# Optimization experiments

Hardware: AMD Instinct MI355X
Metric: run time of the kernel (lower is better)

The kernel has to match this reference:

```python
import jax, jax.numpy as jnp
import numpy as np

E = 8          # n_routed_experts
TOP_K = 2      # num_experts_per_tok
H = 1024       # hidden_size
I = 512        # moe_intermediate_size
SI = 512       # shared expert intermediate (I * n_shared_experts)
B, S = 4, 4096


def setup_inputs() -> dict:
    key = jax.random.key(0)
    ks = jax.random.split(key, 8)
    sc_h = 1.0 / np.sqrt(H)
    sc_i = 1.0 / np.sqrt(I)
    return {
        "hidden_states": jax.random.normal(ks[0], (B, S, H), jnp.float32),
        "gate_w": jax.random.normal(ks[1], (E, H), jnp.float32) * sc_h,  # router logits weight [E,H]
        "Wg": jax.random.normal(ks[2], (E, H, I), jnp.float32) * sc_h,   # per-expert gate_proj
        "Wu": jax.random.normal(ks[3], (E, H, I), jnp.float32) * sc_h,   # per-expert up_proj
        "Wd": jax.random.normal(ks[4], (E, I, H), jnp.float32) * sc_i,   # per-expert down_proj
        "sWg": jax.random.normal(ks[5], (H, SI), jnp.float32) * sc_h,    # shared expert gate_proj
        "sWu": jax.random.normal(ks[6], (H, SI), jnp.float32) * sc_h,
        "sWd": jax.random.normal(ks[7], (SI, H), jnp.float32) * sc_i,
    }


def reference(hidden_states, gate_w, Wg, Wu, Wd, sWg, sWu, sWd):
    b, s, h = hidden_states.shape
    x = hidden_states.reshape(-1, h)                      # [T,H]

    # ---- MoEGate: softmax scoring + greedy top-k + weight normalization ----
    logits = x.astype(jnp.float32) @ gate_w.T             # [T,E]
    scores = jax.nn.softmax(logits, axis=-1)
    topk_w, topk_idx = jax.lax.top_k(scores, TOP_K)       # [T,K]
    topk_w = topk_w / (topk_w.sum(-1, keepdims=True) + 1e-20)  # norm_topk_prob

    # combine weights as a dense [T,E] map (scatter of topk weights)
    cw = (jax.nn.one_hot(topk_idx, E, dtype=topk_w.dtype) * topk_w[..., None]).sum(1)  # [T,E]

    # ---- routed experts: down(gelu(gate(x)) * up(x)), combined by gate weight ----
    g = jnp.einsum("th,ehi->tei", x, Wg)
    u = jnp.einsum("th,ehi->tei", x, Wu)
    inter = jax.nn.gelu(g, approximate=False) * u         # [T,E,I]
    y = jnp.einsum("tei,te,eih->th", inter, cw.astype(x.dtype), Wd)

    # ---- shared expert on the identity path ----
    sh = (jax.nn.gelu(x @ sWg, approximate=False) * (x @ sWu)) @ sWd

    return (y + sh).reshape(b, s, h)
```

## Files before the change

kernel.cpp:

```cpp
#include <hip/hip_runtime.h>
#include <hip/hip_bf16.h>
#include <math.h>


#define T_TOTAL 16384
#define HDIM 1024
#define IDIM 512
#define NE 9
#define CNT_STRIDE 16

typedef __bf16 bf16x8 __attribute__((ext_vector_type(8)));
typedef float f32x4 __attribute__((ext_vector_type(4)));

typedef __attribute__((address_space(1))) void gvoid_t;
typedef __attribute__((address_space(3))) void lvoid_t;

__device__ __forceinline__ void load_lds16(const void* g, void* l) {
  __builtin_amdgcn_global_load_lds((const gvoid_t*)g, (lvoid_t*)l, 16, 0, 0);
}

__device__ __forceinline__ f32x4 mfma_bf16(bf16x8 a, bf16x8 b, f32x4 c) {
  return __builtin_amdgcn_mfma_f32_16x16x32_bf16(a, b, c, 0, 0, 0);
}

__global__ __launch_bounds__(256) void k_gate(const float* __restrict__ x,
                                              const float* __restrict__ gw,
                                              __bf16* __restrict__ xb,
                                              int* __restrict__ tok,
                                              float* __restrict__ wtl,
                                              int* __restrict__ cnt) {
  __shared__ int s_eid[64][2];
  __shared__ float s_wt[64][2];
  __shared__ int s_rank[64][2];
  __shared__ int lcnt[8];
  __shared__ int lbase[8];
  const int wv = threadIdx.x >> 6, lane = threadIdx.x & 63;
  if (threadIdx.x < 8) lcnt[threadIdx.x] = 0;
  __syncthreads();

  for (int i = 0; i < 16; i++) {
    const int tl = wv * 16 + i;
    const int t = blockIdx.x * 64 + tl;
    const float* xr = x + (size_t)t * HDIM + lane * 16;
    float4 xv[4];
#pragma unroll
    for (int j = 0; j < 4; j++) xv[j] = ((const float4*)xr)[j];

    bf16x8 v0, v1;
#pragma unroll
    for (int j = 0; j < 8; j++) v0[j] = (__bf16)((const float*)xv)[j];
#pragma unroll
    for (int j = 0; j < 8; j++) v1[j] = (__bf16)((const float*)xv)[j + 8];
    bf16x8* xbo = (bf16x8*)(xb + (size_t)t * HDIM + lane * 16);
    xbo[0] = v0;
    xbo[1] = v1;

    float acc[8];
#pragma unroll
    for (int e = 0; e < 8; e++) {
      const float4* gp = (const float4*)(gw + e * HDIM + lane * 16);
      float s = 0.f;
#pragma unroll
      for (int j = 0; j < 4; j++) {
        float4 g = gp[j];
        s += xv[j].x * g.x + xv[j].y * g.y + xv[j].z * g.z + xv[j].w * g.w;
      }
      acc[e] = s;
    }
#pragma unroll
    for (int d = 32; d >= 1; d >>= 1) {
#pragma unroll
      for (int e = 0; e < 8; e++) acc[e] += __shfl_xor(acc[e], d, 64);
    }
    if (lane == 0) {
      float mx = acc[0];
#pragma unroll
      for (int e = 1; e < 8; e++) mx = fmaxf(mx, acc[e]);
      float p[8], Z = 0.f;
#pragma unroll
      for (int e = 0; e < 8; e++) {
        p[e] = expf(acc[e] - mx);
        Z += p[e];
      }
#pragma unroll
      for (int e = 0; e < 8; e++) p[e] /= Z;
      int i1 = 0;
#pragma unroll
      for (int e = 1; e < 8; e++)
        if (p[e] > p[i1]) i1 = e;
      int i2 = (i1 == 0) ? 1 : 0;
#pragma unroll
      for (int e = 0; e < 8; e++)
        if (e != i1 && p[e] > p[i2]) i2 = e;
      const float s12 = p[i1] + p[i2] + 1e-20f;
      s_eid[tl][0] = i1;
      s_eid[tl][1] = i2;
      s_wt[tl][0] = p[i1] / s12;
      s_wt[tl][1] = p[i2] / s12;
    }
  }
  __syncthreads();

  if (threadIdx.x < 64) {
    s_rank[threadIdx.x][0] = atomicAdd(&lcnt[s_eid[threadIdx.x][0]], 1);
    s_rank[threadIdx.x][1] = atomicAdd(&lcnt[s_eid[threadIdx.x][1]], 1);
  }
  __syncthreads();
  if (threadIdx.x < 8)
    lbase[threadIdx.x] =
        atomicAdd(&cnt[threadIdx.x * CNT_STRIDE], lcnt[threadIdx.x]);
  __syncthreads();
  if (threadIdx.x < 64) {
    const int t = blockIdx.x * 64 + threadIdx.x;
#pragma unroll
    for (int j = 0; j < 2; j++) {
      const int e = s_eid[threadIdx.x][j];
      const int slot = lbase[e] + s_rank[threadIdx.x][j];
      tok[e * T_TOTAL + slot] = t;
      wtl[e * T_TOTAL + slot] = s_wt[threadIdx.x][j];
    }
  }
}

__global__ __launch_bounds__(256) void k_transpose(const float* __restrict__ w8,
                                                   const float* __restrict__ w1,
                                                   __bf16* __restrict__ out,
                                                   int R, int C) {
  __shared__ float tile[32][33];
  const int b = blockIdx.z;
  const float* src = (b < 8) ? (w8 + (size_t)b * R * C) : w1;
  const int c0 = blockIdx.x * 32, r0 = blockIdx.y * 32;
  const int tx = threadIdx.x & 31, ty = threadIdx.x >> 5;
#pragma unroll
  for (int i = 0; i < 4; i++)
    tile[ty + i * 8][tx] = src[(size_t)(r0 + ty + i * 8) * C + c0 + tx];
  __syncthreads();
#pragma unroll
  for (int i = 0; i < 4; i++)
    out[(size_t)b * R * C + (size_t)(c0 + ty + i * 8) * R + r0 + tx] =
        (__bf16)tile[tx][ty + i * 8];
}

__global__ __launch_bounds__(256) void k_transpose_fuse(
    const float* __restrict__ w8, const float* __restrict__ w1,
    __bf16* __restrict__ out, int u16off) {
  __shared__ float tile[32][33];
  const int b = blockIdx.z;
  const float* src = (b < 8) ? (w8 + (size_t)b * HDIM * IDIM) : w1;
  const int c0 = blockIdx.x * 32, r0 = blockIdx.y * 32;
  const int tx = threadIdx.x & 31, ty = threadIdx.x >> 5;
#pragma unroll
  for (int i = 0; i < 4; i++)
    tile[ty + i * 8][tx] = src[(size_t)(r0 + ty + i * 8) * IDIM + c0 + tx];
  __syncthreads();
#pragma unroll
  for (int i = 0; i < 4; i++) {
    const int ic = c0 + ty + i * 8;
    const int f = 2 * (ic & ~15) + (ic & 15) + u16off;
    out[(size_t)b * 1024 * HDIM + (size_t)f * HDIM + r0 + tx] =
        (__bf16)tile[tx][ty + i * 8];
  }
}

__global__ __launch_bounds__(256, 2) void k_gu(
    const __bf16* __restrict__ xb, const __bf16* __restrict__ Wfu,
    const int* __restrict__ tok, const float* __restrict__ wtl,
    const int* __restrict__ cnt, __bf16* __restrict__ inter) {
  const int e = blockIdx.z;
  const bool se = (e == 8);
  const int cnt_e = se ? T_TOTAL : cnt[e * CNT_STRIDE];
  const int m0 = blockIdx.x * 128;
  if (m0 >= cnt_e) return;

  __shared__ __bf16 sA[128][64];
  __shared__ __bf16 sB[128][64];
  const int tid = threadIdx.x, w = tid >> 6, lane = tid & 63;
  const int n0 = blockIdx.y * 128;
  const int quad = lane >> 4, l16 = lane & 15;
  const int wm = (w & 1) * 64, wn = (w >> 1) * 64;

  const int sr = tid >> 3;
  const int scs = ((tid & 7) ^ (sr & 7)) * 8;
  const __bf16* ap[4];
  const __bf16* bp[4];
#pragma unroll
  for (int sh = 0; sh < 4; sh++) {
    int s = m0 + sh * 32 + sr;
    if (s > cnt_e - 1) s = cnt_e - 1;
    const int t = se ? s : tok[e * T_TOTAL + s];
    ap[sh] = xb + (size_t)t * HDIM + scs;
    bp[sh] = Wfu + ((size_t)e * 1024 + n0 + sh * 32 + sr) * HDIM + scs;
  }
  char* const la = (char*)sA + w * 1024;
  char* const lb = (char*)sB + w * 1024;

  f32x4 acc[4][4];
#pragma unroll
  for (int im = 0; im < 4; im++)
#pragma unroll
    for (int in = 0; in < 4; in++) acc[im][in] = {0.f, 0.f, 0.f, 0.f};

  for (int k = 0; k < HDIM; k += 64) {
    __syncthreads();
#pragma unroll
    for (int sh = 0; sh < 4; sh++) {
      load_lds16(ap[sh], la + sh * 4096);
      load_lds16(bp[sh], lb + sh * 4096);
      ap[sh] += 64;
      bp[sh] += 64;
    }
    __syncthreads();
#pragma unroll
    for (int kh = 0; kh < 2; kh++) {
      bf16x8 af[4], bfr[4];
#pragma unroll
      for (int i = 0; i < 4; i++) {
        const int ra = wm + i * 16 + l16;
        af[i] = *(const bf16x8*)((const char*)sA + ra * 128 +
                                 ((kh * 4 + quad) ^ (ra & 7)) * 16);
        const int rb = wn + i * 16 + l16;
        bfr[i] = *(const bf16x8*)((const char*)sB + rb * 128 +
                                  ((kh * 4 + quad) ^ (rb & 7)) * 16);
      }
#pragma unroll
      for (int im = 0; im < 4; im++)
#pragma unroll
        for (int in = 0; in < 4; in++)
          acc[im][in] = mfma_bf16(af[im], bfr[in], acc[im][in]);
    }
  }

#pragma unroll
  for (int im = 0; im < 4; im++) {
#pragma unroll
    for (int r = 0; r < 4; r++) {
      const int slot = m0 + wm + im * 16 + quad * 4 + r;
      if (slot < cnt_e) {
        const float wt = se ? 1.0f : wtl[e * T_TOTAL + slot];
        __bf16* op =
            inter + ((size_t)e * T_TOTAL + slot) * IDIM + ((n0 + wn) >> 1) + l16;
#pragma unroll
        for (int p = 0; p < 2; p++) {
          const float g = acc[im][2 * p][r];
          const float u = acc[im][2 * p + 1][r];
          const float v =
              wt * u * 0.5f * g * (1.0f + erff(g * 0.70710678118654752f));
          op[p * 16] = (__bf16)v;
        }
      }
    }
  }
}

__global__ __launch_bounds__(256, 2) void k_down_s(const __bf16* __restrict__ iA,
                                                   const __bf16* __restrict__ wB,
                                                   float* __restrict__ out) {
  __shared__ __bf16 sA[128][64];
  __shared__ __bf16 sB[128][64];
  const int tid = threadIdx.x, w = tid >> 6, lane = tid & 63;
  const int m0 = blockIdx.x * 128, n0 = blockIdx.y * 128;
  const int quad = lane >> 4, l16 = lane & 15;
  const int wm = (w & 1) * 64, wn = (w >> 1) * 64;

  const int sr = tid >> 3;
  const int scs = ((tid & 7) ^ (sr & 7)) * 8;
  const __bf16* ap[4];
  const __bf16* bp[4];
#pragma unroll
  for (int sh = 0; sh < 4; sh++) {
    ap[sh] = iA + (size_t)(m0 + sh * 32 + sr) * IDIM + scs;
    bp[sh] = wB + (size_t)(n0 + sh * 32 + sr) * IDIM + scs;
  }
  char* const la = (char*)sA + w * 1024;
  char* const lb = (char*)sB + w * 1024;

  f32x4 acc[4][4];
#pragma unroll
  for (int im = 0; im < 4; im++)
#pragma unroll
    for (int in = 0; in < 4; in++) acc[im][in] = {0.f, 0.f, 0.f, 0.f};

  for (int k = 0; k < IDIM; k += 64) {
    __syncthreads();
#pragma unroll
    for (int sh = 0; sh < 4; sh++) {
      load_lds16(ap[sh], la + sh * 4096);
      load_lds16(bp[sh], lb + sh * 4096);
      ap[sh] += 64;
      bp[sh] += 64;
    }
    __syncthreads();
#pragma unroll
    for (int kh = 0; kh < 2; kh++) {
      bf16x8 af[4], bfr[4];
#pragma unroll
      for (int i = 0; i < 4; i++) {
        const int ra = wm + i * 16 + l16;
        af[i] = *(const bf16x8*)((const char*)sA + ra * 128 +
                                 ((kh * 4 + quad) ^ (ra & 7)) * 16);
        const int rb = wn + i * 16 + l16;
        bfr[i] = *(const bf16x8*)((const char*)sB + rb * 128 +
                                  ((kh * 4 + quad) ^ (rb & 7)) * 16);
      }
#pragma unroll
      for (int im = 0; im < 4; im++)
#pragma unroll
        for (int in = 0; in < 4; in++)
          acc[im][in] = mfma_bf16(af[im], bfr[in], acc[im][in]);
    }
  }

#pragma unroll
  for (int im = 0; im < 4; im++) {
#pragma unroll
    for (int r = 0; r < 4; r++) {
      const int t = m0 + wm + im * 16 + quad * 4 + r;
#pragma unroll
      for (int in = 0; in < 4; in++)
        out[(size_t)t * HDIM + n0 + wn + in * 16 + l16] = acc[im][in][r];
    }
  }
}

__global__ __launch_bounds__(256, 2) void k_down_r(
    const __bf16* __restrict__ inter, const __bf16* __restrict__ WdT,
    const int* __restrict__ tok, const int* __restrict__ cnt,
    float* __restrict__ out) {
  const int e = blockIdx.z;
  const int cnt_e = cnt[e * CNT_STRIDE];
  const int m0 = blockIdx.x * 128;
  if (m0 >= cnt_e) return;

  __shared__ __bf16 sA[128][64];
  __shared__ __bf16 sB[128][64];
  const int tid = threadIdx.x, w = tid >> 6, lane = tid & 63;
  const int n0 = blockIdx.y * 128;
  const int quad = lane >> 4, l16 = lane & 15;
  const int wm = (w & 1) * 64, wn = (w >> 1) * 64;

  const int sr = tid >> 3;
  const int scs = ((tid & 7) ^ (sr & 7)) * 8;
  const __bf16* ap[4];
  const __bf16* bp[4];
#pragma unroll
  for (int sh = 0; sh < 4; sh++) {
    int s = m0 + sh * 32 + sr;
    if (s > cnt_e - 1) s = cnt_e - 1;
    ap[sh] = inter + ((size_t)e * T_TOTAL + s) * IDIM + scs;
    bp[sh] = WdT + ((size_t)e * HDIM + n0 + sh * 32 + sr) * IDIM + scs;
  }
  char* const la = (char*)sA + w * 1024;
  char* const lb = (char*)sB + w * 1024;

  f32x4 acc[4][4];
#pragma unroll
  for (int im = 0; im < 4; im++)
#pragma unroll
    for (int in = 0; in < 4; in++) acc[im][in] = {0.f, 0.f, 0.f, 0.f};

  for (int k = 0; k < IDIM; k += 64) {
    __syncthreads();
#pragma unroll
    for (int sh = 0; sh < 4; sh++) {
      load_lds16(ap[sh], la + sh * 4096);
      load_lds16(bp[sh], lb + sh * 4096);
      ap[sh] += 64;
      bp[sh] += 64;
    }
    __syncthreads();
#pragma unroll
    for (int kh = 0; kh < 2; kh++) {
      bf16x8 af[4], bfr[4];
#pragma unroll
      for (int i = 0; i < 4; i++) {
        const int ra = wm + i * 16 + l16;
        af[i] = *(const bf16x8*)((const char*)sA + ra * 128 +
                                 ((kh * 4 + quad) ^ (ra & 7)) * 16);
        const int rb = wn + i * 16 + l16;
        bfr[i] = *(const bf16x8*)((const char*)sB + rb * 128 +
                                  ((kh * 4 + quad) ^ (rb & 7)) * 16);
      }
#pragma unroll
      for (int im = 0; im < 4; im++)
#pragma unroll
        for (int in = 0; in < 4; in++)
          acc[im][in] = mfma_bf16(af[im], bfr[in], acc[im][in]);
    }
  }

#pragma unroll
  for (int im = 0; im < 4; im++) {
#pragma unroll
    for (int r = 0; r < 4; r++) {
      const int slot = m0 + wm + im * 16 + quad * 4 + r;
      if (slot < cnt_e) {
        const int t = tok[e * T_TOTAL + slot];
#pragma unroll
        for (int in = 0; in < 4; in++)
          atomicAdd(&out[(size_t)t * HDIM + n0 + wn + in * 16 + l16],
                    acc[im][in][r]);
      }
    }
  }
}

extern "C" void kernel_launch(void* const* d_in, const int* in_sizes, int n_in,
                              void* d_out, int out_size, void* d_ws,
                              size_t ws_size, hipStream_t stream) {
  const float* x = (const float*)d_in[0];
  const float* gw = (const float*)d_in[1];
  const float* Wg = (const float*)d_in[2];
  const float* Wu = (const float*)d_in[3];
  const float* Wd = (const float*)d_in[4];
  const float* sWg = (const float*)d_in[5];
  const float* sWu = (const float*)d_in[6];
  const float* sWd = (const float*)d_in[7];
  float* out = (float*)d_out;

  char* ws = (char*)d_ws;
  size_t off = 0;
  auto alloc = [&](size_t n) {
    char* p = ws + off;
    off += (n + 255) & ~(size_t)255;
    return p;
  };
  __bf16* xb = (__bf16*)alloc((size_t)T_TOTAL * HDIM * 2);
  __bf16* Wfu = (__bf16*)alloc((size_t)NE * 1024 * HDIM * 2);
  __bf16* WdT = (__bf16*)alloc((size_t)NE * HDIM * IDIM * 2);
  int* tok = (int*)alloc((size_t)8 * T_TOTAL * 4);
  float* wtl = (float*)alloc((size_t)8 * T_TOTAL * 4);
  int* cnt = (int*)alloc(8 * CNT_STRIDE * 4);
  __bf16* inter = (__bf16*)alloc((size_t)NE * T_TOTAL * IDIM * 2);

  hipMemsetAsync(cnt, 0, 8 * CNT_STRIDE * 4, stream);

  k_gate<<<dim3(T_TOTAL / 64), dim3(256), 0, stream>>>(x, gw, xb, tok, wtl,
                                                       cnt);
  k_transpose_fuse<<<dim3(IDIM / 32, HDIM / 32, NE), dim3(256), 0, stream>>>(
      Wg, sWg, Wfu, 0);
  k_transpose_fuse<<<dim3(IDIM / 32, HDIM / 32, NE), dim3(256), 0, stream>>>(
      Wu, sWu, Wfu, 16);
  k_transpose<<<dim3(HDIM / 32, IDIM / 32, NE), dim3(256), 0, stream>>>(
      Wd, sWd, WdT, IDIM, HDIM);

  k_gu<<<dim3(T_TOTAL / 128, 1024 / 128, NE), dim3(256), 0, stream>>>(
      xb, Wfu, tok, wtl, cnt, inter);

  k_down_s<<<dim3(T_TOTAL / 128, HDIM / 128), dim3(256), 0, stream>>>(
      inter + (size_t)8 * T_TOTAL * IDIM, WdT + (size_t)8 * HDIM * IDIM, out);
  k_down_r<<<dim3(T_TOTAL / 128, HDIM / 128, 8), dim3(256), 0, stream>>>(
      inter, WdT, tok, cnt, out);
}
```

Baseline: 487.0 us.

## Rewrite gate/up GEMM with 256x256 tiles and 4-stage async LDS pipeline

The fused gate/up expert GEMM now uses 512-thread blocks computing 256x256 output tiles with K-step 32. A four-buffer global-to-LDS ring keeps two stages of loads in flight, waited on with explicit vmcnt and raw barriers instead of a full sync around each K step. It also adds setprio around the MFMA bursts and a new swizzle for the paired-row layout. This targets global memory latency stalls and improves operand reuse per block. In exchange it needs 128KB of LDS per block, which limits occupancy, and routed experts with few tokens waste more work in partially filled 256-row tiles.

After: 570.5 us. 1.17x slower.

```diff
diff --git a/kernel.cpp b/kernel.cpp
--- a/kernel.cpp
+++ b/kernel.cpp
@@ -162,87 +162,132 @@
   }
 }
 
-__global__ __launch_bounds__(256, 2) void k_gu(
+__global__ __launch_bounds__(512, 2) void k_gu(
     const __bf16* __restrict__ xb, const __bf16* __restrict__ Wfu,
     const int* __restrict__ tok, const float* __restrict__ wtl,
     const int* __restrict__ cnt, __bf16* __restrict__ inter) {
   const int e = blockIdx.z;
   const bool se = (e == 8);
   const int cnt_e = se ? T_TOTAL : cnt[e * CNT_STRIDE];
-  const int m0 = blockIdx.x * 128;
+  const int m0 = blockIdx.x * 256;
   if (m0 >= cnt_e) return;
 
-  __shared__ __bf16 sA[128][64];
-  __shared__ __bf16 sB[128][64];
-  const int tid = threadIdx.x, w = tid >> 6, lane = tid & 63;
-  const int n0 = blockIdx.y * 128;
+  __shared__ char ldsA[65536];
+  __shared__ char ldsB[65536];
+
+  const int tid = threadIdx.x;
+  const int w = tid >> 6, lane = tid & 63;
   const int quad = lane >> 4, l16 = lane & 15;
-  const int wm = (w & 1) * 64, wn = (w >> 1) * 64;
-
-  const int sr = tid >> 3;
-  const int scs = ((tid & 7) ^ (sr & 7)) * 8;
-  const __bf16* ap[4];
-  const __bf16* bp[4];
-#pragma unroll
-  for (int sh = 0; sh < 4; sh++) {
-    int s = m0 + sh * 32 + sr;
-    if (s > cnt_e - 1) s = cnt_e - 1;
-    const int t = se ? s : tok[e * T_TOTAL + s];
-    ap[sh] = xb + (size_t)t * HDIM + scs;
-    bp[sh] = Wfu + ((size_t)e * 1024 + n0 + sh * 32 + sr) * HDIM + scs;
-  }
-  char* const la = (char*)sA + w * 1024;
-  char* const lb = (char*)sB + w * 1024;
-
-  f32x4 acc[4][4];
-#pragma unroll
-  for (int im = 0; im < 4; im++)
-#pragma unroll
-    for (int in = 0; in < 4; in++) acc[im][in] = {0.f, 0.f, 0.f, 0.f};
-
-  for (int k = 0; k < HDIM; k += 64) {
-    __syncthreads();
-#pragma unroll
-    for (int sh = 0; sh < 4; sh++) {
-      load_lds16(ap[sh], la + sh * 4096);
-      load_lds16(bp[sh], lb + sh * 4096);
-      ap[sh] += 64;
-      bp[sh] += 64;
-    }
-    __syncthreads();
-#pragma unroll
-    for (int kh = 0; kh < 2; kh++) {
-      bf16x8 af[4], bfr[4];
-#pragma unroll
-      for (int i = 0; i < 4; i++) {
-        const int ra = wm + i * 16 + l16;
-        af[i] = *(const bf16x8*)((const char*)sA + ra * 128 +
-                                 ((kh * 4 + quad) ^ (ra & 7)) * 16);
-        const int rb = wn + i * 16 + l16;
-        bfr[i] = *(const bf16x8*)((const char*)sB + rb * 128 +
-                                  ((kh * 4 + quad) ^ (rb & 7)) * 16);
-      }
-#pragma unroll
-      for (int im = 0; im < 4; im++)
-#pragma unroll
-        for (int in = 0; in < 4; in++)
-          acc[im][in] = mfma_bf16(af[im], bfr[in], acc[im][in]);
-    }
-  }
-
-#pragma unroll
-  for (int im = 0; im < 4; im++) {
-#pragma unroll
-    for (int r = 0; r < 4; r++) {
-      const int slot = m0 + wm + im * 16 + quad * 4 + r;
+  const int wm = (w & 1) * 128, wn = (w >> 1) * 64;
+  const int n0 = blockIdx.y * 256;
+  const int wofs = w * 1024;
+
+  const int ln = tid >> 3;
+  const int sp = (tid & 7) ^ (ln & 7);
+  const int r0 = sp >> 2, ccol = sp & 3;
+
+  const __bf16* apc0;
+  const __bf16* apc1;
+  const __bf16* bpc0;
+  const __bf16* bpc1;
+  {
+    int s0 = m0 + 2 * ln + r0;
+    if (s0 > cnt_e - 1) s0 = cnt_e - 1;
+    int s1 = m0 + 128 + 2 * ln + r0;
+    if (s1 > cnt_e - 1) s1 = cnt_e - 1;
+    const int t0 = se ? s0 : tok[e * T_TOTAL + s0];
+    const int t1 = se ? s1 : tok[e * T_TOTAL + s1];
+    apc0 = xb + (size_t)t0 * HDIM + ccol * 8;
+    apc1 = xb + (size_t)t1 * HDIM + ccol * 8;
+    bpc0 = Wfu + ((size_t)e * 1024 + n0 + 2 * ln + r0) * HDIM + ccol * 8;
+    bpc1 = Wfu + ((size_t)e * 1024 + n0 + 128 + 2 * ln + r0) * HDIM + ccol * 8;
+  }
+
+  f32x4 acc[8][4];
+#pragma unroll
+  for (int m = 0; m < 8; m++)
+#pragma unroll
+    for (int n = 0; n < 4; n++) acc[m][n] = {0.f, 0.f, 0.f, 0.f};
+
+  auto stage = [&](int tt) {
+    char* dA = ldsA + (tt & 3) * 16384 + wofs;
+    char* dB = ldsB + (tt & 3) * 16384 + wofs;
+    load_lds16(apc0, dA);
+    load_lds16(apc1, dA + 8192);
+    load_lds16(bpc0, dB);
+    load_lds16(bpc1, dB + 8192);
+    apc0 += 32;
+    apc1 += 32;
+    bpc0 += 32;
+    bpc1 += 32;
+  };
+
+  const int so16 = ((((l16 & 1) << 2) + quad) ^ (l16 >> 1)) * 16;
+
+  auto compute = [&](int tt) {
+    const char* bA = ldsA + (tt & 3) * 16384;
+    const char* bB = ldsB + (tt & 3) * 16384;
+    bf16x8 bfr[4], af[4];
+#pragma unroll
+    for (int n = 0; n < 4; ++n) {
+      const int j = (wn + n * 16 + l16) >> 1;
+      bfr[n] = *(const bf16x8*)(bB + j * 128 + so16);
+    }
+#pragma unroll
+    for (int m = 0; m < 4; ++m) {
+      const int j = (wm + m * 16 + l16) >> 1;
+      af[m] = *(const bf16x8*)(bA + j * 128 + so16);
+    }
+    __builtin_amdgcn_s_setprio(1);
+#pragma unroll
+    for (int m = 0; m < 4; ++m)
+#pragma unroll
+      for (int n = 0; n < 4; ++n)
+        acc[m][n] = mfma_bf16(af[m], bfr[n], acc[m][n]);
+    __builtin_amdgcn_s_setprio(0);
+    __builtin_amdgcn_s_barrier();
+#pragma unroll
+    for (int m = 0; m < 4; ++m) {
+      const int j = (wm + 64 + m * 16 + l16) >> 1;
+      af[m] = *(const bf16x8*)(bA + j * 128 + so16);
+    }
+    __builtin_amdgcn_s_setprio(1);
+#pragma unroll
+    for (int m = 0; m < 4; ++m)
+#pragma unroll
+      for (int n = 0; n < 4; ++n)
+        acc[4 + m][n] = mfma_bf16(af[m], bfr[n], acc[4 + m][n]);
+    __builtin_amdgcn_s_setprio(0);
+  };
+
+  stage(0);
+  stage(1);
+  for (int t = 0; t < 30; ++t) {
+    stage(t + 2);
+    asm volatile("s_waitcnt vmcnt(8)" ::: "memory");
+    __builtin_amdgcn_s_barrier();
+    compute(t);
+  }
+  asm volatile("s_waitcnt vmcnt(4)" ::: "memory");
+  __builtin_amdgcn_s_barrier();
+  compute(30);
+  asm volatile("s_waitcnt vmcnt(0)" ::: "memory");
+  __builtin_amdgcn_s_barrier();
+  compute(31);
+
+#pragma unroll
+  for (int m = 0; m < 8; ++m) {
+#pragma unroll
+    for (int r = 0; r < 4; ++r) {
+      const int slot = m0 + wm + m * 16 + quad * 4 + r;
       if (slot < cnt_e) {
         const float wt = se ? 1.0f : wtl[e * T_TOTAL + slot];
-        __bf16* op =
-            inter + ((size_t)e * T_TOTAL + slot) * IDIM + ((n0 + wn) >> 1) + l16;
-#pragma unroll
-        for (int p = 0; p < 2; p++) {
-          const float g = acc[im][2 * p][r];
-          const float u = acc[im][2 * p + 1][r];
+        __bf16* op = inter + ((size_t)e * T_TOTAL + slot) * IDIM +
+                     ((n0 + wn) >> 1) + l16;
+#pragma unroll
+        for (int p = 0; p < 2; ++p) {
+          const float g = acc[m][2 * p][r];
+          const float u = acc[m][2 * p + 1][r];
           const float v =
               wt * u * 0.5f * g * (1.0f + erff(g * 0.70710678118654752f));
           op[p * 16] = (__bf16)v;
@@ -443,7 +488,7 @@
   k_transpose<<<dim3(HDIM / 32, IDIM / 32, NE), dim3(256), 0, stream>>>(
       Wd, sWd, WdT, IDIM, HDIM);
 
-  k_gu<<<dim3(T_TOTAL / 128, 1024 / 128, NE), dim3(256), 0, stream>>>(
+  k_gu<<<dim3(T_TOTAL / 256, 1024 / 256, NE), dim3(512), 0, stream>>>(
       xb, Wfu, tok, wtl, cnt, inter);
 
   k_down_s<<<dim3(T_TOTAL / 128, HDIM / 128), dim3(256), 0, stream>>>(
```

## Replace atomic scatter in routed down-proj with dense staging buffer and combine

Applied to the files above, without the earlier changes.

The routed down-projection no longer scatters into the output by token index (likely with atomics). Instead each expert writes its rows contiguously into a staging buffer, placed by per-expert base offsets from a small scan kernel. A new combine kernel then gathers each token's two expert rows through an inverse map and adds them to the shared-expert output. This removes scattered or atomic global writes, at the cost of an extra 128MB fp32 buffer being written and read, plus two more kernel launches. It falls back to the old path if the workspace is too small.

Measured after the change: 501.0 us. +2.9%, slower.

```diff
diff --git a/kernel.cpp b/kernel.cpp
--- a/kernel.cpp
+++ b/kernel.cpp
@@ -28,7 +28,8 @@
                                               __bf16* __restrict__ xb,
                                               int* __restrict__ tok,
                                               float* __restrict__ wtl,
-                                              int* __restrict__ cnt) {
+                                              int* __restrict__ cnt,
+                                              int* __restrict__ inv) {
   __shared__ int s_eid[64][2];
   __shared__ float s_wt[64][2];
   __shared__ int s_rank[64][2];
@@ -118,6 +119,18 @@
       const int slot = lbase[e] + s_rank[threadIdx.x][j];
       tok[e * T_TOTAL + slot] = t;
       wtl[e * T_TOTAL + slot] = s_wt[threadIdx.x][j];
+      inv[t * 2 + j] = e * T_TOTAL + slot;
+    }
+  }
+}
+
+__global__ void k_scan(const int* __restrict__ cnt, int* __restrict__ base) {
+  if (threadIdx.x == 0 && blockIdx.x == 0) {
+    int s = 0;
+#pragma unroll
+    for (int e = 0; e < 8; e++) {
+      base[e] = s;
+      s += cnt[e * CNT_STRIDE];
     }
   }
 }
@@ -319,6 +332,110 @@
       for (int in = 0; in < 4; in++)
         out[(size_t)t * HDIM + n0 + wn + in * 16 + l16] = acc[im][in][r];
     }
+  }
+}
+
+__global__ __launch_bounds__(256, 2) void k_down_rs(
+    const __bf16* __restrict__ inter, const __bf16* __restrict__ WdT,
+    const int* __restrict__ cnt, const int* __restrict__ base,
+    float* __restrict__ yb) {
+  const int e = blockIdx.z;
+  const int cnt_e = cnt[e * CNT_STRIDE];
+  const int m0 = blockIdx.x * 128;
+  if (m0 >= cnt_e) return;
+  const int rowb = base[e];
+
+  __shared__ __bf16 sA[128][64];
+  __shared__ __bf16 sB[128][64];
+  const int tid = threadIdx.x, w = tid >> 6, lane = tid & 63;
+  const int n0 = blockIdx.y * 128;
+  const int quad = lane >> 4, l16 = lane & 15;
+  const int wm = (w & 1) * 64, wn = (w >> 1) * 64;
+
+  const int sr = tid >> 3;
+  const int scs = ((tid & 7) ^ (sr & 7)) * 8;
+  const __bf16* ap[4];
+  const __bf16* bp[4];
+#pragma unroll
+  for (int sh = 0; sh < 4; sh++) {
+    int s = m0 + sh * 32 + sr;
+    if (s > cnt_e - 1) s = cnt_e - 1;
+    ap[sh] = inter + ((size_t)e * T_TOTAL + s) * IDIM + scs;
+    bp[sh] = WdT + ((size_t)e * HDIM + n0 + sh * 32 + sr) * IDIM + scs;
+  }
+  char* const la = (char*)sA + w * 1024;
+  char* const lb = (char*)sB + w * 1024;
+
+  f32x4 acc[4][4];
+#pragma unroll
+  for (int im = 0; im < 4; im++)
+#pragma unroll
+    for (int in = 0; in < 4; in++) acc[im][in] = {0.f, 0.f, 0.f, 0.f};
+
+  for (int k = 0; k < IDIM; k += 64) {
+    __syncthreads();
+#pragma unroll
+    for (int sh = 0; sh < 4; sh++) {
+      load_lds16(ap[sh], la + sh * 4096);
+      load_lds16(bp[sh], lb + sh * 4096);
+      ap[sh] += 64;
+      bp[sh] += 64;
+    }
+    __syncthreads();
+#pragma unroll
+    for (int kh = 0; kh < 2; kh++) {
+      bf16x8 af[4], bfr[4];
+#pragma unroll
+      for (int i = 0; i < 4; i++) {
+        const int ra = wm + i * 16 + l16;
+        af[i] = *(const bf16x8*)((const char*)sA + ra * 128 +
+                                 ((kh * 4 + quad) ^ (ra & 7)) * 16);
+        const int rb = wn + i * 16 + l16;
+        bfr[i] = *(const bf16x8*)((const char*)sB + rb * 128 +
+                                  ((kh * 4 + quad) ^ (rb & 7)) * 16);
+      }
+#pragma unroll
+      for (int im = 0; im < 4; im++)
+#pragma unroll
+        for (int in = 0; in < 4; in++)
+          acc[im][in] = mfma_bf16(af[im], bfr[in], acc[im][in]);
+    }
+  }
+
+#pragma unroll
+  for (int im = 0; im < 4; im++) {
+#pragma unroll
+    for (int r = 0; r < 4; r++) {
+      const int slot = m0 + wm + im * 16 + quad * 4 + r;
+      if (slot < cnt_e) {
+        float* op = yb + (size_t)(rowb + slot) * HDIM + n0 + wn + l16;
+#pragma unroll
+        for (int in = 0; in < 4; in++) op[in * 16] = acc[im][in][r];
+      }
+    }
+  }
+}
+
+__global__ __launch_bounds__(256) void k_combine(const float* __restrict__ yb,
+                                                 const int* __restrict__ inv,
+                                                 const int* __restrict__ base,
+                                                 float* __restrict__ out) {
+  const int t = blockIdx.x * 4 + (threadIdx.x >> 6);
+  const int lane = threadIdx.x & 63;
+  const int v1 = inv[2 * t], v2 = inv[2 * t + 1];
+  const int r1 = base[v1 >> 14] + (v1 & (T_TOTAL - 1));
+  const int r2 = base[v2 >> 14] + (v2 & (T_TOTAL - 1));
+  const float4* y1 = (const float4*)(yb + (size_t)r1 * HDIM);
+  const float4* y2 = (const float4*)(yb + (size_t)r2 * HDIM);
+  float4* o = (float4*)(out + (size_t)t * HDIM);
+#pragma unroll
+  for (int j = 0; j < 4; j++) {
+    const int c = lane + j * 64;
+    float4 a = o[c];
+    float4 b = y1[c];
+    float4 d = y2[c];
+    o[c] = make_float4(a.x + b.x + d.x, a.y + b.y + d.y, a.z + b.z + d.z,
+                       a.w + b.w + d.w);
   }
 }
 
@@ -430,24 +547,38 @@
   int* tok = (int*)alloc((size_t)8 * T_TOTAL * 4);
   float* wtl = (float*)alloc((size_t)8 * T_TOTAL * 4);
   int* cnt = (int*)alloc(8 * CNT_STRIDE * 4);
+  int* inv = (int*)alloc((size_t)T_TOTAL * 2 * 4);
+  int* base = (int*)alloc(16 * 4);
   __bf16* inter = (__bf16*)alloc((size_t)NE * T_TOTAL * IDIM * 2);
 
+  const size_t yb_bytes = (size_t)2 * T_TOTAL * HDIM * 4;
+  const bool store_path = (off + yb_bytes) <= ws_size;
+  float* yb = store_path ? (float*)alloc(yb_bytes) : nullptr;
+
   hipMemsetAsync(cnt, 0, 8 * CNT_STRIDE * 4, stream);
 
   k_gate<<<dim3(T_TOTAL / 64), dim3(256), 0, stream>>>(x, gw, xb, tok, wtl,
-                                                       cnt);
+                                                       cnt, inv);
   k_transpose_fuse<<<dim3(IDIM / 32, HDIM / 32, NE), dim3(256), 0, stream>>>(
       Wg, sWg, Wfu, 0);
   k_transpose_fuse<<<dim3(IDIM / 32, HDIM / 32, NE), dim3(256), 0, stream>>>(
       Wu, sWu, Wfu, 16);
   k_transpose<<<dim3(HDIM / 32, IDIM / 32, NE), dim3(256), 0, stream>>>(
       Wd, sWd, WdT, IDIM, HDIM);
+  k_scan<<<dim3(1), dim3(64), 0, stream>>>(cnt, base);
 
   k_gu<<<dim3(T_TOTAL / 128, 1024 / 128, NE), dim3(256), 0, stream>>>(
       xb, Wfu, tok, wtl, cnt, inter);
 
   k_down_s<<<dim3(T_TOTAL / 128, HDIM / 128), dim3(256), 0, stream>>>(
       inter + (size_t)8 * T_TOTAL * IDIM, WdT + (size_t)8 * HDIM * IDIM, out);
-  k_down_r<<<dim3(T_TOTAL / 128, HDIM / 128, 8), dim3(256), 0, stream>>>(
-      inter, WdT, tok, cnt, out);
-}
+
+  if (store_path) {
+    k_down_rs<<<dim3(T_TOTAL / 128, HDIM / 128, 8), dim3(256), 0, stream>>>(
+        inter, WdT, cnt, base, yb);
+    k_combine<<<dim3(T_TOTAL / 4), dim3(256), 0, stream>>>(yb, inv, base, out);
+  } else {
+    k_down_r<<<dim3(T_TOTAL / 128, HDIM / 128, 8), dim3(256), 0, stream>>>(
+        inter, WdT, tok, cnt, out);
+  }
+}
```
